# Optimization experiments

Hardware: AMD Instinct MI355X
Metric: run time of the kernel (lower is better)

Reference implementation:

```python
import jax, jax.numpy as jnp
import numpy as np

FP8_MAX = 448.0
EPS = 1e-12
SCALE_MARGIN = 0.9


def _fp8_quant(t, scale):
    # clamp to e4m3 range, round-trip through float8_e4m3fn to emulate fp8 storage
    q = jnp.clip(t * scale, -FP8_MAX, FP8_MAX)
    return q.astype(jnp.float8_e4m3fn).astype(jnp.float32)


def setup_inputs() -> dict:
    key = jax.random.key(0)
    k1, k2, k3 = jax.random.split(key, 3)
    B, S, K, N = 4, 4096, 2048, 2048
    x = jax.random.normal(k1, (B, S, K), dtype=jnp.float32)
    # kaiming_uniform_(a=sqrt(5)) => U(-1/sqrt(K), 1/sqrt(K)) bound approx; emulate with uniform
    bound_w = 1.0 / np.sqrt(K)
    weight = jax.random.uniform(k2, (N, K), minval=-bound_w, maxval=bound_w, dtype=jnp.float32)
    bound_b = 1.0 / np.sqrt(K)
    bias = jax.random.uniform(k3, (N,), minval=-bound_b, maxval=bound_b, dtype=jnp.float32)
    return {"x": x, "weight": weight, "bias": bias}


def reference(x, weight, bias):
    in_features = weight.shape[1]
    out_features = weight.shape[0]
    # dynamic per-tensor scales (amax history starts at zero -> max == current amax);
    # torch computes these via .item() on buffers => no gradient
    input_scale = jax.lax.stop_gradient(FP8_MAX / (jnp.max(jnp.abs(x)) + EPS) * SCALE_MARGIN)
    weight_scale = jax.lax.stop_gradient(FP8_MAX / (jnp.max(jnp.abs(weight)) + EPS) * SCALE_MARGIN)
    x_fp8 = _fp8_quant(x, input_scale)          # [B, S, K] (fp8-rounded values in fp32)
    w_fp8 = _fp8_quant(weight, weight_scale)    # [N, K]
    out = jnp.matmul(x_fp8.reshape(-1, in_features), w_fp8.T)  # [B*S, N] in fp32
    out = out / (input_scale * weight_scale)
    out = out.reshape(*x.shape[:-1], out_features).astype(x.dtype)
    return out + bias
```

## Files before the change

kernel.cpp:

```cpp
#include <hip/hip_runtime.h>
#include <hip/hip_cooperative_groups.h>

namespace cg = cooperative_groups;


typedef __attribute__((ext_vector_type(4))) float floatx4;
typedef __attribute__((ext_vector_type(4))) int intx4;
typedef __attribute__((ext_vector_type(8))) int intx8;

#define FP8_MAX_F 448.0f
#define SIDE_GRID 1024

__device__ __forceinline__ void async_load16(const void* g, void* l) {
    __builtin_amdgcn_global_load_lds(
        (const __attribute__((address_space(1))) unsigned int*)g,
        (__attribute__((address_space(3))) unsigned int*)l,
        16, 0, 0);
}

__device__ __forceinline__ float scale_from_amax_f(float a) {
    return FP8_MAX_F / (a + 1e-12f) * 0.9f;
}
__device__ __forceinline__ float scale_from_amax(unsigned int bits) {
    return scale_from_amax_f(__uint_as_float(bits));
}

__global__ __launch_bounds__(256) void amax_quant(
    const float* __restrict__ x, long xn4,
    const float* __restrict__ w, long wn4,
    float* __restrict__ partials,
    unsigned int* __restrict__ amax,
    unsigned int* __restrict__ xq,
    unsigned int* __restrict__ wq) {
    const float4* xv = (const float4*)x;
    const float4* wv = (const float4*)w;
    const long tid = (long)blockIdx.x * 256 + threadIdx.x;
    const long stride = (long)SIDE_GRID * 256;
    const int lane = threadIdx.x & 63, wid = threadIdx.x >> 6;
    __shared__ float red[2][4];

    float mx = 0.0f, mw = 0.0f;
    for (long j = tid; j < xn4; j += stride) {
        float4 v = xv[j];
        mx = fmaxf(mx, fmaxf(fmaxf(fabsf(v.x), fabsf(v.y)),
                             fmaxf(fabsf(v.z), fabsf(v.w))));
    }
    for (long j = tid; j < wn4; j += stride) {
        float4 v = wv[j];
        mw = fmaxf(mw, fmaxf(fmaxf(fabsf(v.x), fabsf(v.y)),
                             fmaxf(fabsf(v.z), fabsf(v.w))));
    }
    #pragma unroll
    for (int off = 32; off > 0; off >>= 1) {
        mx = fmaxf(mx, __shfl_down(mx, off));
        mw = fmaxf(mw, __shfl_down(mw, off));
    }
    if (lane == 0) { red[0][wid] = mx; red[1][wid] = mw; }
    __syncthreads();
    if (threadIdx.x == 0) {
        partials[blockIdx.x] =
            fmaxf(fmaxf(red[0][0], red[0][1]), fmaxf(red[0][2], red[0][3]));
        partials[SIDE_GRID + blockIdx.x] =
            fmaxf(fmaxf(red[1][0], red[1][1]), fmaxf(red[1][2], red[1][3]));
    }

    cg::this_grid().sync();

    mx = 0.0f; mw = 0.0f;
    for (int p = threadIdx.x; p < SIDE_GRID; p += 256) {
        mx = fmaxf(mx, partials[p]);
        mw = fmaxf(mw, partials[SIDE_GRID + p]);
    }
    #pragma unroll
    for (int off = 32; off > 0; off >>= 1) {
        mx = fmaxf(mx, __shfl_down(mx, off));
        mw = fmaxf(mw, __shfl_down(mw, off));
    }
    if (lane == 0) { red[0][wid] = mx; red[1][wid] = mw; }
    __syncthreads();
    mx = fmaxf(fmaxf(red[0][0], red[0][1]), fmaxf(red[0][2], red[0][3]));
    mw = fmaxf(fmaxf(red[1][0], red[1][1]), fmaxf(red[1][2], red[1][3]));
    if (blockIdx.x == 0 && threadIdx.x == 0) {
        amax[0] = __float_as_uint(mx);
        amax[1] = __float_as_uint(mw);
    }

    const float sx = scale_from_amax_f(mx);
    const float sw = scale_from_amax_f(mw);
    for (long j = tid; j < xn4; j += stride) {
        float4 v = xv[j];
        float a0 = fminf(fmaxf(v.x * sx, -FP8_MAX_F), FP8_MAX_F);
        float a1 = fminf(fmaxf(v.y * sx, -FP8_MAX_F), FP8_MAX_F);
        float a2 = fminf(fmaxf(v.z * sx, -FP8_MAX_F), FP8_MAX_F);
        float a3 = fminf(fmaxf(v.w * sx, -FP8_MAX_F), FP8_MAX_F);
        int p = __builtin_amdgcn_cvt_pk_fp8_f32(a0, a1, 0, false);
        p = __builtin_amdgcn_cvt_pk_fp8_f32(a2, a3, p, true);
        xq[j] = (unsigned int)p;
    }
    for (long j = tid; j < wn4; j += stride) {
        float4 v = wv[j];
        float a0 = fminf(fmaxf(v.x * sw, -FP8_MAX_F), FP8_MAX_F);
        float a1 = fminf(fmaxf(v.y * sw, -FP8_MAX_F), FP8_MAX_F);
        float a2 = fminf(fmaxf(v.z * sw, -FP8_MAX_F), FP8_MAX_F);
        float a3 = fminf(fmaxf(v.w * sw, -FP8_MAX_F), FP8_MAX_F);
        int p = __builtin_amdgcn_cvt_pk_fp8_f32(a0, a1, 0, false);
        p = __builtin_amdgcn_cvt_pk_fp8_f32(a2, a3, p, true);
        wq[j] = (unsigned int)p;
    }
}

#define BM 128
#define BN 128
#define BKB 128

__global__ __launch_bounds__(256, 3) void gemm_fp8mx(
    const unsigned char* __restrict__ A,
    const unsigned char* __restrict__ B,
    const float* __restrict__ bias,
    const unsigned int* __restrict__ amax,
    float* __restrict__ C,
    int M, int N, int K) {
    __shared__ __align__(16) unsigned char As[BM * BKB];
    __shared__ __align__(16) unsigned char Bs[BN * BKB];

    const int t = threadIdx.x;
    const int lane = t & 63;
    const int w = t >> 6;

    int flat = blockIdx.y * gridDim.x + blockIdx.x;
    const int nwg = gridDim.x * gridDim.y;
    if ((nwg & 7) == 0) flat = (flat & 7) * (nwg >> 3) + (flat >> 3);
    const int bm = (flat / gridDim.x) * BM;
    const int bn = (flat % gridDim.x) * BN;

    const int wm = (w >> 1) * 64;
    const int wn = (w & 1) * 64;

    floatx4 acc[4][4] = {};

    const int srow = t >> 3;
    const int gcol = ((t & 7) ^ (srow & 7)) * 16;
    const unsigned char* gA = A + (long)(bm + srow) * K + gcol;
    const unsigned char* gB = B + (long)(bn + srow) * K + gcol;
    unsigned char* lA = As + t * 16;
    unsigned char* lB = Bs + t * 16;

    const int fr = lane & 15;
    const int sw = fr & 7;
    const int b0 = (lane >> 4) * 2;
    const int off0 = (b0 ^ sw) * 16;
    const int off1 = ((b0 + 1) ^ sw) * 16;
    const int rowA = (wm + fr) * BKB;
    const int rowB = (wn + fr) * BKB;

    for (int kt = 0; kt < K; kt += BKB) {
        __syncthreads();
        #pragma unroll
        for (int c = 0; c < 4; c++) {
            async_load16(gA + (long)c * 32 * K + kt, lA + c * 4096);
            async_load16(gB + (long)c * 32 * K + kt, lB + c * 4096);
        }
        __syncthreads();

        intx8 bfrag[4];
        #pragma unroll
        for (int j = 0; j < 4; j++) {
            intx4 lo = *(const intx4*)(Bs + rowB + j * 2048 + off0);
            intx4 hi = *(const intx4*)(Bs + rowB + j * 2048 + off1);
            bfrag[j] = (intx8){lo.x, lo.y, lo.z, lo.w, hi.x, hi.y, hi.z, hi.w};
        }
        #pragma unroll
        for (int i = 0; i < 4; i++) {
            intx4 lo = *(const intx4*)(As + rowA + i * 2048 + off0);
            intx4 hi = *(const intx4*)(As + rowA + i * 2048 + off1);
            intx8 afrag = (intx8){lo.x, lo.y, lo.z, lo.w, hi.x, hi.y, hi.z, hi.w};
            #pragma unroll
            for (int j = 0; j < 4; j++)
                acc[i][j] = __builtin_amdgcn_mfma_scale_f32_16x16x128_f8f6f4(
                    afrag, bfrag[j], acc[i][j],
                     0,  0,
                    0, 0x7f7f7f7f, 0, 0x7f7f7f7f);
        }
    }

    const float is = scale_from_amax(amax[0]);
    const float ws = scale_from_amax(amax[1]);
    const float rcp = 1.0f / (is * ws);
    const int crow = bm + wm + (lane >> 4) * 4;
    const int ccol = bn + wn + fr;
    #pragma unroll
    for (int j = 0; j < 4; j++) {
        const int col = ccol + j * 16;
        const float bv = bias[col];
        #pragma unroll
        for (int i = 0; i < 4; i++) {
            const int row0 = crow + i * 16;
            #pragma unroll
            for (int r = 0; r < 4; r++)
                __builtin_nontemporal_store(acc[i][j][r] * rcp + bv,
                                            &C[(long)(row0 + r) * N + col]);
        }
    }
}

extern "C" void kernel_launch(void* const* d_in, const int* in_sizes, int n_in,
                              void* d_out, int out_size, void* d_ws, size_t ws_size,
                              hipStream_t stream) {
    const float* x = (const float*)d_in[0];
    const float* wt = (const float*)d_in[1];
    const float* bias = (const float*)d_in[2];
    float* out = (float*)d_out;

    const int xn = in_sizes[0];
    const int wn = in_sizes[1];
    const int N = in_sizes[2];
    const int K = wn / N;
    const int M = xn / K;

    unsigned char* wsb = (unsigned char*)d_ws;
    unsigned int* amax = (unsigned int*)wsb;
    unsigned char* xq = wsb + 64;
    unsigned char* wq = wsb + 64 + (size_t)xn;

    float* partials = out;
    long xn4 = (long)xn / 4, wn4 = (long)wn / 4;
    const float* xa = x;
    const float* wa = wt;
    unsigned int* xqa = (unsigned int*)xq;
    unsigned int* wqa = (unsigned int*)wq;
    void* kargs[] = {(void*)&xa, (void*)&xn4, (void*)&wa, (void*)&wn4,
                     (void*)&partials, (void*)&amax, (void*)&xqa, (void*)&wqa};
    hipLaunchCooperativeKernel((void*)amax_quant, dim3(SIDE_GRID), dim3(256),
                               kargs, 0, stream);

    dim3 grid(N / BN, M / BM);
    gemm_fp8mx<<<grid, 256, 0, stream>>>(xq, wq, bias, amax, out, M, N, K);
}
```

Measured before the change: 430.0 us.

## Split cooperative amax-quant kernel into two regular launches, drop nontemporal stores

Replaces the single cooperative kernel, which used a grid-wide sync between the amax reduction and quantisation, with two ordinary kernels: one writes per-block partial maxima and the other reduces them and quantises. The grid grows to 2048 blocks, the partials move from the output buffer into the workspace, and loop unroll pragmas are added. The GEMM epilogue also switches from nontemporal stores to plain stores. The aim is to avoid cooperative launch overhead and the grid barrier, at the cost of an extra launch and every quant block re-reducing all partials.

```diff
diff --git a/kernel.cpp b/kernel.cpp
--- a/kernel.cpp
+++ b/kernel.cpp
@@ -1,7 +1,4 @@
 #include <hip/hip_runtime.h>
-#include <hip/hip_cooperative_groups.h>
-
-namespace cg = cooperative_groups;
 
 
 typedef __attribute__((ext_vector_type(4))) float floatx4;
@@ -9,7 +6,7 @@
 typedef __attribute__((ext_vector_type(8))) int intx8;
 
 #define FP8_MAX_F 448.0f
-#define SIDE_GRID 1024
+#define SGRID 2048
 
 __device__ __forceinline__ void async_load16(const void* g, void* l) {
     __builtin_amdgcn_global_load_lds(
@@ -25,26 +22,23 @@
     return scale_from_amax_f(__uint_as_float(bits));
 }
 
-__global__ __launch_bounds__(256) void amax_quant(
+__global__ __launch_bounds__(256) void amax_partial(
     const float* __restrict__ x, long xn4,
     const float* __restrict__ w, long wn4,
-    float* __restrict__ partials,
-    unsigned int* __restrict__ amax,
-    unsigned int* __restrict__ xq,
-    unsigned int* __restrict__ wq) {
+    float* __restrict__ partials) {
     const float4* xv = (const float4*)x;
     const float4* wv = (const float4*)w;
     const long tid = (long)blockIdx.x * 256 + threadIdx.x;
-    const long stride = (long)SIDE_GRID * 256;
-    const int lane = threadIdx.x & 63, wid = threadIdx.x >> 6;
-    __shared__ float red[2][4];
+    const long stride = (long)SGRID * 256;
 
     float mx = 0.0f, mw = 0.0f;
+    #pragma unroll 4
     for (long j = tid; j < xn4; j += stride) {
         float4 v = xv[j];
         mx = fmaxf(mx, fmaxf(fmaxf(fabsf(v.x), fabsf(v.y)),
                              fmaxf(fabsf(v.z), fabsf(v.w))));
     }
+    #pragma unroll 2
     for (long j = tid; j < wn4; j += stride) {
         float4 v = wv[j];
         mw = fmaxf(mw, fmaxf(fmaxf(fabsf(v.x), fabsf(v.y)),
@@ -55,27 +49,37 @@
         mx = fmaxf(mx, __shfl_down(mx, off));
         mw = fmaxf(mw, __shfl_down(mw, off));
     }
+    __shared__ float red[2][4];
+    const int lane = threadIdx.x & 63, wid = threadIdx.x >> 6;
     if (lane == 0) { red[0][wid] = mx; red[1][wid] = mw; }
     __syncthreads();
     if (threadIdx.x == 0) {
         partials[blockIdx.x] =
             fmaxf(fmaxf(red[0][0], red[0][1]), fmaxf(red[0][2], red[0][3]));
-        partials[SIDE_GRID + blockIdx.x] =
+        partials[SGRID + blockIdx.x] =
             fmaxf(fmaxf(red[1][0], red[1][1]), fmaxf(red[1][2], red[1][3]));
     }
-
-    cg::this_grid().sync();
-
-    mx = 0.0f; mw = 0.0f;
-    for (int p = threadIdx.x; p < SIDE_GRID; p += 256) {
+}
+
+__global__ __launch_bounds__(256) void quant_both(
+    const float* __restrict__ x, long xn4,
+    const float* __restrict__ w, long wn4,
+    const float* __restrict__ partials,
+    unsigned int* __restrict__ amax,
+    unsigned int* __restrict__ xq,
+    unsigned int* __restrict__ wq) {
+    float mx = 0.0f, mw = 0.0f;
+    for (int p = threadIdx.x; p < SGRID; p += 256) {
         mx = fmaxf(mx, partials[p]);
-        mw = fmaxf(mw, partials[SIDE_GRID + p]);
+        mw = fmaxf(mw, partials[SGRID + p]);
     }
     #pragma unroll
     for (int off = 32; off > 0; off >>= 1) {
         mx = fmaxf(mx, __shfl_down(mx, off));
         mw = fmaxf(mw, __shfl_down(mw, off));
     }
+    __shared__ float red[2][4];
+    const int lane = threadIdx.x & 63, wid = threadIdx.x >> 6;
     if (lane == 0) { red[0][wid] = mx; red[1][wid] = mw; }
     __syncthreads();
     mx = fmaxf(fmaxf(red[0][0], red[0][1]), fmaxf(red[0][2], red[0][3]));
@@ -87,6 +91,11 @@
 
     const float sx = scale_from_amax_f(mx);
     const float sw = scale_from_amax_f(mw);
+    const float4* xv = (const float4*)x;
+    const float4* wv = (const float4*)w;
+    const long tid = (long)blockIdx.x * 256 + threadIdx.x;
+    const long stride = (long)SGRID * 256;
+    #pragma unroll 2
     for (long j = tid; j < xn4; j += stride) {
         float4 v = xv[j];
         float a0 = fminf(fmaxf(v.x * sx, -FP8_MAX_F), FP8_MAX_F);
@@ -97,6 +106,7 @@
         p = __builtin_amdgcn_cvt_pk_fp8_f32(a2, a3, p, true);
         xq[j] = (unsigned int)p;
     }
+    #pragma unroll 2
     for (long j = tid; j < wn4; j += stride) {
         float4 v = wv[j];
         float a0 = fminf(fmaxf(v.x * sw, -FP8_MAX_F), FP8_MAX_F);
@@ -197,8 +207,7 @@
             const int row0 = crow + i * 16;
             #pragma unroll
             for (int r = 0; r < 4; r++)
-                __builtin_nontemporal_store(acc[i][j][r] * rcp + bv,
-                                            &C[(long)(row0 + r) * N + col]);
+                C[(long)(row0 + r) * N + col] = acc[i][j][r] * rcp + bv;
         }
     }
 }
@@ -219,20 +228,14 @@
 
     unsigned char* wsb = (unsigned char*)d_ws;
     unsigned int* amax = (unsigned int*)wsb;
-    unsigned char* xq = wsb + 64;
-    unsigned char* wq = wsb + 64 + (size_t)xn;
-
-    float* partials = out;
+    float* partials = (float*)(wsb + 64);
+    unsigned char* xq = wsb + 64 + 2 * SGRID * 4;
+    unsigned char* wq = xq + (size_t)xn;
+
     long xn4 = (long)xn / 4, wn4 = (long)wn / 4;
-    const float* xa = x;
-    const float* wa = wt;
-    unsigned int* xqa = (unsigned int*)xq;
-    unsigned int* wqa = (unsigned int*)wq;
-    void* kargs[] = {(void*)&xa, (void*)&xn4, (void*)&wa, (void*)&wn4,
-                     (void*)&partials, (void*)&amax, (void*)&xqa, (void*)&wqa};
-    hipLaunchCooperativeKernel((void*)amax_quant, dim3(SIDE_GRID), dim3(256),
-                               kargs, 0, stream);
-
+    amax_partial<<<SGRID, 256, 0, stream>>>(x, xn4, wt, wn4, partials);
+    quant_both<<<SGRID, 256, 0, stream>>>(x, xn4, wt, wn4, partials, amax,
+                                          (unsigned int*)xq, (unsigned int*)wq);
     dim3 grid(N / BN, M / BM);
     gemm_fp8mx<<<grid, 256, 0, stream>>>(xq, wq, bias, amax, out, M, N, K);
 }
```

Result: faster. 356.3 us (-17.2%).
